# Performance work log

Hardware: AMD Instinct MI355X
Metric: run time of the kernel (lower is better)

Reference implementation:

```python
import jax, jax.numpy as jnp
import numpy as np

B, S, D, H = 1, 2048, 4096, 32
HD = D // H
THETA = 10000.0
IN_SCALE = 0.1   # input_scale buffer
Q_SCALE = 0.1    # q_proj_scale buffer
K_SCALE = 0.1    # k_proj_scale buffer
V_SCALE = 0.1    # v_proj_scale buffer
OUT_SCALE = 0.1  # out_input_scale buffer


def _fake_q(x, scale, lo, hi):
    # round-to-int + clamp, kept in float (faithful to int8 fake-quant)
    return jnp.clip(jnp.round(x / scale), lo, hi)


def _w4a8_linear(x, qw, w_scale, in_scale):
    # int8 fake-quantized activation x int4-valued weight, dequant output
    qx = _fake_q(x, in_scale, -128, 127)
    return jnp.einsum('bsd,od->bso', qx, qw) * (in_scale * w_scale)


def _rope_tables(position_ids):
    inv_freq = 1.0 / (THETA ** (jnp.arange(0, HD, 2, dtype=jnp.float32) / HD))
    ang = position_ids.astype(jnp.float32)[..., None] * inv_freq  # [B,S,HD/2]
    emb = jnp.concatenate([ang, ang], axis=-1)                     # [B,S,HD]
    return jnp.cos(emb)[:, None], jnp.sin(emb)[:, None]            # [B,1,S,HD]


def _rotate_half(x):
    return jnp.concatenate([-x[..., HD // 2:], x[..., :HD // 2]], axis=-1)


def setup_inputs() -> dict:
    key = jax.random.key(0)
    ks = jax.random.split(key, 9)
    hidden_states = jax.random.normal(ks[0], (B, S, D), jnp.float32)
    def int4_w(k):
        return jnp.round(jax.random.uniform(k, (D, D), jnp.float32, -8.0, 7.0))
    def ch_scale(k):
        return jax.random.uniform(k, (D,), jnp.float32, 0.01, 0.03)
    wq, wk, wv, wo = int4_w(ks[1]), int4_w(ks[2]), int4_w(ks[3]), int4_w(ks[4])
    sq_w, sk_w, sv_w, so_w = ch_scale(ks[5]), ch_scale(ks[6]), ch_scale(ks[7]), ch_scale(ks[8])
    position_ids = jnp.arange(S, dtype=jnp.int32)[None, :]
    causal = jnp.tril(jnp.ones((S, S), dtype=bool))
    attention_mask = jnp.where(causal, 0.0, -1e9).astype(jnp.float32)[None, None]
    return dict(hidden_states=hidden_states, wq=wq, wk=wk, wv=wv, wo=wo,
                sq_w=sq_w, sk_w=sk_w, sv_w=sv_w, so_w=so_w,
                attention_mask=attention_mask, position_ids=position_ids)


def reference(hidden_states, wq, wk, wv, wo, sq_w, sk_w, sv_w, so_w,
              attention_mask, position_ids):
    # W4A8 dequant projections
    q = _w4a8_linear(hidden_states, wq, sq_w, IN_SCALE)
    k = _w4a8_linear(hidden_states, wk, sk_w, IN_SCALE)
    v = _w4a8_linear(hidden_states, wv, sv_w, IN_SCALE)
    q = q.reshape(B, S, H, HD).transpose(0, 2, 1, 3)  # [B,H,S,HD]
    k = k.reshape(B, S, H, HD).transpose(0, 2, 1, 3)
    v = v.reshape(B, S, H, HD).transpose(0, 2, 1, 3)
    # RoPE
    cos, sin = _rope_tables(position_ids)
    q = q * cos + _rotate_half(q) * sin
    k = k * cos + _rotate_half(k) * sin
    # int8 fake-quant of q/k/v, then dequant before matmuls
    q = _fake_q(q, Q_SCALE, -128, 127)
    k = _fake_q(k, K_SCALE, -128, 127)
    v = _fake_q(v, V_SCALE, -128, 127)
    scores = jnp.einsum('bhqd,bhkd->bhqk', q * Q_SCALE, k * K_SCALE) / np.sqrt(HD)
    scores = scores + attention_mask
    attn = jax.nn.softmax(scores.astype(jnp.float32), axis=-1)
    out = jnp.einsum('bhqk,bhkd->bhqd', attn, v * V_SCALE)
    out = out.transpose(0, 2, 1, 3).reshape(B, S, D)
    # o_proj input re-quantized to int8 with out_input_scale (clamp -127..127)
    out_q = _fake_q(out, OUT_SCALE, -127, 127)
    attn_output = jnp.einsum('bsd,od->bso', out_q, wo) * (OUT_SCALE * so_w)
    return attn_output
```

## Files before the change

### kernel.cpp

```cpp
#include <hip/hip_runtime.h>
#include <math.h>
#include <stdint.h>

#define S_LEN 2048
#define D_DIM 4096
#define NHEAD 32
#define HDIM  128

typedef int      v4i __attribute__((ext_vector_type(4)));
typedef float    v4f __attribute__((ext_vector_type(4)));
typedef _Float16 v8h __attribute__((ext_vector_type(8)));

__device__ __forceinline__ float quant128(float x) {
  return fminf(fmaxf(rintf(x / 0.1f), -128.f), 127.f);
}
__device__ __forceinline__ void gl_lds16(const void* g, void* l) {
  __builtin_amdgcn_global_load_lds(
      (const __attribute__((address_space(1))) void*)g,
      (__attribute__((address_space(3))) void*)l, 16, 0, 0);
}

__global__ __launch_bounds__(256) void quant_hidden_k(const float* __restrict__ in,
                                                      int8_t* __restrict__ out) {
  const int idx = blockIdx.x * 256 + threadIdx.x;
  const float4 v = ((const float4*)in)[idx];
  const int q0 = (int)quant128(v.x), q1 = (int)quant128(v.y);
  const int q2 = (int)quant128(v.z), q3 = (int)quant128(v.w);
  ((int*)out)[idx] = (q0 & 0xff) | ((q1 & 0xff) << 8) | ((q2 & 0xff) << 16) | ((q3 & 0xff) << 24);
}

__global__ __launch_bounds__(256) void wconv3_k(const float* __restrict__ a,
                                                const float* __restrict__ b,
                                                const float* __restrict__ c,
                                                int8_t* __restrict__ out) {
  const int which = blockIdx.x >> 14;
  const int sub = blockIdx.x & 16383;
  const float* src = (which == 0) ? a : (which == 1) ? b : c;
  const int idx = sub * 256 + threadIdx.x;
  const float4 v = ((const float4*)src)[idx];
  const int q0 = __float2int_rn(v.x), q1 = __float2int_rn(v.y);
  const int q2 = __float2int_rn(v.z), q3 = __float2int_rn(v.w);
  ((int*)out)[(size_t)which * 4194304 + idx] =
      (q0 & 0xff) | ((q1 & 0xff) << 8) | ((q2 & 0xff) << 16) | ((q3 & 0xff) << 24);
}

__global__ __launch_bounds__(256) void wconv_k(const float* __restrict__ in,
                                               int8_t* __restrict__ out) {
  const int idx = blockIdx.x * 256 + threadIdx.x;
  const float4 v = ((const float4*)in)[idx];
  const int q0 = __float2int_rn(v.x), q1 = __float2int_rn(v.y);
  const int q2 = __float2int_rn(v.z), q3 = __float2int_rn(v.w);
  ((int*)out)[idx] = (q0 & 0xff) | ((q1 & 0xff) << 8) | ((q2 & 0xff) << 16) | ((q3 & 0xff) << 24);
}

__global__ __launch_bounds__(256) void rope_tab_k(const int* __restrict__ pos,
                                                  float* __restrict__ ct,
                                                  float* __restrict__ st) {
  const int idx = blockIdx.x * 256 + threadIdx.x;
  const int s = idx >> 6, j = idx & 63;
  const float inv = exp2f((float)j * -0.20762050593046016f);
  const float a = (float)pos[s] * inv;
  float si, c;
  sincosf(a, &si, &c);
  ct[idx] = c;
  st[idx] = si;
}

template <int MODE>
__device__ __forceinline__ void gemm_body(
    int8_t* __restrict__ LS, const int8_t* __restrict__ A8,
    const int8_t* __restrict__ W8, const float* __restrict__ s0,
    const float* __restrict__ s1, const float* __restrict__ s2,
    const float* __restrict__ ctab, const float* __restrict__ stab,
    void* __restrict__ out0, void* __restrict__ out1, void* __restrict__ out2,
    int nwg) {
  int8_t* const Abase = LS;
  int8_t* const Bbase = LS + 49152;

  const int t = threadIdx.x;
  const int w = t >> 6, lane = t & 63, g = lane >> 4, l15 = lane & 15;
  const int wm = w >> 2, wn = w & 3;

  const int bid = blockIdx.x;
  const int lb = (bid & 7) * (nwg >> 3) + (bid >> 3);
  const int within = lb & 15, g16 = lb >> 4;
  const int bm = ((g16 & 3) * 4 + (within >> 2)) * 128;
  const int bn = ((g16 >> 2) * 4 + (within & 3)) * 256;

  const int rowo = lane >> 3;
  const int schunk = ((lane & 7) ^ rowo) * 16;
  const int8_t* srcA[2];
  const int8_t* srcB[4];
#pragma unroll
  for (int i = 0; i < 2; ++i)
    srcA[i] = A8 + (size_t)(bm + w * 16 + i * 8 + rowo) * D_DIM + schunk;
#pragma unroll
  for (int i = 0; i < 4; ++i)
    srcB[i] = W8 + (size_t)(bn + w * 32 + i * 8 + rowo) * D_DIM + schunk;

#define STAGE(KT, BI)                                                       \
  {                                                                         \
    const int kof_ = (KT) * 128;                                            \
    int8_t* Ad_ = Abase + (BI) * 16384 + w * 2048;                          \
    int8_t* Bd_ = Bbase + (BI) * 32768 + w * 4096;                          \
    _Pragma("unroll") for (int i_ = 0; i_ < 2; ++i_)                        \
        gl_lds16(srcA[i_] + kof_, Ad_ + i_ * 1024);                         \
    _Pragma("unroll") for (int i_ = 0; i_ < 4; ++i_)                        \
        gl_lds16(srcB[i_] + kof_, Bd_ + i_ * 1024);                         \
  }

  const int nc0 = (wn & 1) * 32 + (wn >> 1) * 128;

  const int coff0 = (g ^ (l15 & 7)) * 16;
  const int coff1 = ((4 | g) ^ (l15 & 7)) * 16;
  const int aoff = (wm * 64 + l15) * 128;
  int boff[4];
#pragma unroll
  for (int ni = 0; ni < 4; ++ni)
    boff[ni] = (nc0 + (ni & 1) * 16 + (ni >> 1) * 64 + l15) * 128;

  v4i fa[4], fb[4];
  v4i ga[4], gb[4];

#define RD(FA, FB, BI, COFF)                                                \
  {                                                                         \
    const int8_t* Ab_ = Abase + (BI) * 16384;                               \
    const int8_t* Bb_ = Bbase + (BI) * 32768;                               \
    _Pragma("unroll") for (int mi_ = 0; mi_ < 4; ++mi_)                     \
        FA[mi_] = *(const v4i*)(Ab_ + aoff + mi_ * 2048 + (COFF));          \
    _Pragma("unroll") for (int ni_ = 0; ni_ < 4; ++ni_)                     \
        FB[ni_] = *(const v4i*)(Bb_ + boff[ni_] + (COFF));                  \
  }

#define MM(FA, FB)                                                          \
  _Pragma("unroll") for (int mi_ = 0; mi_ < 4; ++mi_)                       \
  _Pragma("unroll") for (int ni_ = 0; ni_ < 4; ++ni_)                       \
      acc[mi_][ni_] = __builtin_amdgcn_mfma_i32_16x16x64_i8(                \
          FA[mi_], FB[ni_], acc[mi_][ni_], 0, 0, 0);

  v4i acc[4][4];
#pragma unroll
  for (int mi = 0; mi < 4; ++mi)
#pragma unroll
    for (int ni = 0; ni < 4; ++ni) acc[mi][ni] = (v4i){0, 0, 0, 0};

  STAGE(0, 0)
  STAGE(1, 1)
  asm volatile("s_waitcnt vmcnt(6)" ::: "memory");
  __builtin_amdgcn_s_barrier();
  __builtin_amdgcn_sched_barrier(0);
  RD(fa, fb, 0, coff0)

  for (int t3 = 0; t3 < 33; t3 += 3) {
#pragma unroll
    for (int u = 0; u < 3; ++u) {
      const int kt = t3 + u;
      if (kt < 32) {
        if (kt + 2 < 32) STAGE(kt + 2, ((u + 2) % 3))
        RD(ga, gb, u, coff1)
        __builtin_amdgcn_s_setprio(1);
        MM(fa, fb)
        MM(ga, gb)
        __builtin_amdgcn_s_setprio(0);
        if (kt + 2 < 32)
          asm volatile("s_waitcnt vmcnt(6)" ::: "memory");
        else
          asm volatile("s_waitcnt vmcnt(0)" ::: "memory");
        __builtin_amdgcn_s_barrier();
        __builtin_amdgcn_sched_barrier(0);
        if (kt + 1 < 32) RD(fa, fb, ((u + 1) % 3), coff0)
      }
    }
  }
#undef STAGE
#undef RD
#undef MM

  const int srow0 = bm + wm * 64;
  if (MODE == 1) {
    float* dst = (float*)out0;
#pragma unroll
    for (int ni = 0; ni < 4; ++ni) {
      const int col = bn + nc0 + (ni & 1) * 16 + (ni >> 1) * 64 + l15;
      const float sc = 0.1f * s0[col];
#pragma unroll
      for (int mi = 0; mi < 4; ++mi)
#pragma unroll
        for (int r = 0; r < 4; ++r)
          dst[(size_t)(srow0 + mi * 16 + g * 4 + r) * D_DIM + col] =
              (float)acc[mi][ni][r] * sc;
    }
  } else {
    const int seg = bn >> 12;
    const int bcol = bn & 4095;
    if (seg == 2) {
      _Float16* dst = (_Float16*)out2;
#pragma unroll
      for (int ni = 0; ni < 4; ++ni) {
        const int col = bcol + nc0 + (ni & 1) * 16 + (ni >> 1) * 64 + l15;
        const float scv = 0.1f * s2[col];
#pragma unroll
        for (int mi = 0; mi < 4; ++mi)
#pragma unroll
          for (int r = 0; r < 4; ++r) {
            const int s = srow0 + mi * 16 + g * 4 + r;
            dst[(size_t)col * S_LEN + s] = (_Float16)quant128((float)acc[mi][ni][r] * scv);
          }
      }
    } else {
      const float* wsc = seg ? s1 : s0;
      int8_t* dst = seg ? (int8_t*)out1 : (int8_t*)out0;
      const int hb = bcol + (wn >> 1) * 128;
#pragma unroll
      for (int ni = 0; ni < 2; ++ni) {
        const int dlo = (wn & 1) * 32 + ni * 16 + l15;
        const int clo = hb + dlo;
        const float sc0 = 0.1f * wsc[clo];
        const float sc1 = 0.1f * wsc[clo + 64];
#pragma unroll
        for (int mi = 0; mi < 4; ++mi)
#pragma unroll
          for (int r = 0; r < 4; ++r) {
            const int s = srow0 + mi * 16 + g * 4 + r;
            const float c = ctab[s * 64 + dlo];
            const float si = stab[s * 64 + dlo];
            const float x1 = (float)acc[mi][ni][r] * sc0;
            const float x2 = (float)acc[mi][ni + 2][r] * sc1;
            dst[(size_t)s * D_DIM + clo] = (int8_t)quant128(x1 * c - x2 * si);
            dst[(size_t)s * D_DIM + clo + 64] = (int8_t)quant128(x2 * c + x1 * si);
          }
      }
    }
  }
}

__global__ __launch_bounds__(512) void gemm_qkv(
    const int8_t* __restrict__ A8, const int8_t* __restrict__ W8,
    const float* __restrict__ s0, const float* __restrict__ s1,
    const float* __restrict__ s2, const float* __restrict__ ctab,
    const float* __restrict__ stab, void* __restrict__ out0,
    void* __restrict__ out1, void* __restrict__ out2) {
  __shared__ __align__(16) int8_t LS[3 * 16384 + 3 * 32768];
  gemm_body<0>(LS, A8, W8, s0, s1, s2, ctab, stab, out0, out1, out2, 768);
}

__global__ __launch_bounds__(512) void gemm_out(
    const int8_t* __restrict__ A8, const int8_t* __restrict__ W8,
    const float* __restrict__ s0, const float* __restrict__ ctab,
    const float* __restrict__ stab, void* __restrict__ out0) {
  __shared__ __align__(16) int8_t LS[3 * 16384 + 3 * 32768];
  gemm_body<1>(LS, A8, W8, s0, s0, s0, ctab, stab, out0, out0, out0, 256);
}

__global__ __launch_bounds__(512, 4) void attn_v8(
    const int8_t* __restrict__ q8, const int8_t* __restrict__ k8,
    const _Float16* __restrict__ vT, int8_t* __restrict__ o8) {
  __shared__ __align__(16) int8_t Kls[3][8192];
  __shared__ __align__(16) int8_t Vls[3][16384];
  const int jj = 15 - blockIdx.x;
  const int h = blockIdx.y;
  const int t = threadIdx.x;
  const int w = t >> 6, lane = t & 63, g = lane >> 4, l15 = lane & 15;
  const int T = 2 * jj + 2;
  const int q0 = (jj * 8 + w) * 16;
  const int q_lane = q0 + l15;
  const float SSCALE = 8.838834764831845e-4f;
  const v8h vones = {(_Float16)1, (_Float16)1, (_Float16)1, (_Float16)1,
                     (_Float16)1, (_Float16)1, (_Float16)1, (_Float16)1};

  const int ks_slot = t >> 3;
  const int ks_cs = (t & 7) ^ (ks_slot & 7);
  const int ks_key = ((ks_slot >> 5) & 1) * 32 + ((ks_slot >> 3) & 1) * 16 +
                     ((ks_slot >> 2) & 1) * 8 + ((ks_slot >> 4) & 1) * 4 +
                     (ks_slot & 3);
  const int k_src = ks_key * D_DIM + ks_cs * 16;
  const int k_dst = t * 16;
  int v_src[2], v_dst[2];
#pragma unroll
  for (int i = 0; i < 2; ++i) {
    const int lin = i * 512 + t;
    const int d = lin >> 3;
    const int cs = (lin & 7) ^ (d & 7);
    v_src[i] = d * S_LEN + cs * 8;
    v_dst[i] = lin * 16;
  }
  const int8_t* kbg = k8 + (size_t)h * HDIM;
  const _Float16* vbg = vT + (size_t)h * HDIM * S_LEN;

  auto stage = [&](int kt, int b) {
    const int8_t* ks = kbg + (size_t)kt * (64 * D_DIM);
    const _Float16* vs = vbg + kt * 64;
    gl_lds16(ks + k_src, &Kls[b][k_dst]);
#pragma unroll
    for (int i = 0; i < 2; ++i) gl_lds16(vs + v_src[i], &Vls[b][v_dst[i]]);
  };

  const v4i qa0 = *(const v4i*)(q8 + (size_t)q_lane * D_DIM + h * HDIM + g * 16);
  const v4i qa1 = *(const v4i*)(q8 + (size_t)q_lane * D_DIM + h * HDIM + 64 + g * 16);

  v4f o[8];
#pragma unroll
  for (int n = 0; n < 8; ++n) o[n] = (v4f){0.f, 0.f, 0.f, 0.f};
  v4f lacc = (v4f){0.f, 0.f, 0.f, 0.f};
  float m_i = -INFINITY;

  stage(0, 0);
  if (T > 1) stage(1, 1);

  int bi = 0;
  for (int kt = 0; kt < T; ++kt) {
    if (kt + 1 < T)
      asm volatile("s_waitcnt vmcnt(3)" ::: "memory");
    else
      asm volatile("s_waitcnt vmcnt(0)" ::: "memory");
    __builtin_amdgcn_s_barrier();
    __builtin_amdgcn_sched_barrier(0);
    if (kt + 2 < T) stage(kt + 2, bi >= 1 ? bi - 1 : bi + 2);

    const int ksw = (l15 & 7);
    float sc[4][4];
#pragma unroll
    for (int nt = 0; nt < 4; ++nt) {
      const int8_t* kr = &Kls[bi][(nt * 16 + l15) * 128];
      const v4i kb0 = *(const v4i*)(kr + ((g ^ ksw) * 16));
      const v4i kb1 = *(const v4i*)(kr + (((4 + g) ^ ksw) * 16));
      v4i c = (v4i){0, 0, 0, 0};
      c = __builtin_amdgcn_mfma_i32_16x16x64_i8(kb0, qa0, c, 0, 0, 0);
      c = __builtin_amdgcn_mfma_i32_16x16x64_i8(kb1, qa1, c, 0, 0, 0);
#pragma unroll
      for (int r = 0; r < 4; ++r) {
        float s = (float)c[r] * SSCALE;
        if (kt >= T - 2) {
          const int key = kt * 64 + ((nt >> 1) << 5) + ((g >> 1) << 4) +
                          ((g & 1) << 3) + ((nt & 1) << 2) + r;
          if (key > q_lane) s = -1.0e30f;
        }
        sc[nt][r] = s;
      }
    }
    float mx = fmaxf(fmaxf(fmaxf(sc[0][0], sc[0][1]), fmaxf(sc[0][2], sc[0][3])),
                     fmaxf(fmaxf(sc[1][0], sc[1][1]), fmaxf(sc[1][2], sc[1][3])));
    mx = fmaxf(mx, fmaxf(fmaxf(fmaxf(sc[2][0], sc[2][1]), fmaxf(sc[2][2], sc[2][3])),
                         fmaxf(fmaxf(sc[3][0], sc[3][1]), fmaxf(sc[3][2], sc[3][3]))));
    mx = fmaxf(mx, __shfl_xor(mx, 16));
    mx = fmaxf(mx, __shfl_xor(mx, 32));
    const float mnew = fmaxf(m_i, mx);
    const float alpha = __expf(m_i - mnew);
    m_i = mnew;

    float p[4][4];
#pragma unroll
    for (int nt = 0; nt < 4; ++nt)
#pragma unroll
      for (int r = 0; r < 4; ++r) p[nt][r] = __expf(sc[nt][r] - m_i);

    v8h ph0, ph1;
#pragma unroll
    for (int e = 0; e < 8; ++e) {
      ph0[e] = (_Float16)p[e >> 2][e & 3];
      ph1[e] = (_Float16)p[2 + (e >> 2)][e & 3];
    }
    float a_r[4];
#pragma unroll
    for (int r = 0; r < 4; ++r)
      a_r[r] = __shfl(alpha, (lane & 48) | (g * 4 + r));
#pragma unroll
    for (int n = 0; n < 8; ++n)
#pragma unroll
      for (int r = 0; r < 4; ++r) o[n][r] *= a_r[r];
#pragma unroll
    for (int r = 0; r < 4; ++r) lacc[r] *= a_r[r];

    __builtin_amdgcn_s_setprio(1);
    lacc = __builtin_amdgcn_mfma_f32_16x16x32_f16(ph0, vones, lacc, 0, 0, 0);
    lacc = __builtin_amdgcn_mfma_f32_16x16x32_f16(ph1, vones, lacc, 0, 0, 0);
#pragma unroll
    for (int nt = 0; nt < 8; ++nt) {
      const int8_t* vr = &Vls[bi][(nt * 16 + l15) * 128];
      const v8h v0 = *(const v8h*)(vr + ((g ^ ksw) * 16));
      const v8h v1 = *(const v8h*)(vr + (((4 + g) ^ ksw) * 16));
      o[nt] = __builtin_amdgcn_mfma_f32_16x16x32_f16(ph0, v0, o[nt], 0, 0, 0);
      o[nt] = __builtin_amdgcn_mfma_f32_16x16x32_f16(ph1, v1, o[nt], 0, 0, 0);
    }
    __builtin_amdgcn_s_setprio(0);

    bi = (bi == 2) ? 0 : bi + 1;
  }

#pragma unroll
  for (int r = 0; r < 4; ++r) {
    const float rL = 1.0f / lacc[r];
    const size_t row = (size_t)(q0 + g * 4 + r) * D_DIM + h * HDIM;
#pragma unroll
    for (int nt = 0; nt < 8; ++nt) {
      const int q = (int)fminf(fmaxf(rintf(o[nt][r] * rL), -127.f), 127.f);
      o8[row + nt * 16 + l15] = (int8_t)q;
    }
  }
}

extern "C" void kernel_launch(void* const* d_in, const int* in_sizes, int n_in,
                              void* d_out, int out_size, void* d_ws, size_t ws_size,
                              hipStream_t stream) {
  (void)in_sizes; (void)n_in; (void)out_size; (void)ws_size;
  const float* hidden = (const float*)d_in[0];
  const float* wq = (const float*)d_in[1];
  const float* wk = (const float*)d_in[2];
  const float* wv = (const float*)d_in[3];
  const float* wo = (const float*)d_in[4];
  const float* sq = (const float*)d_in[5];
  const float* sk = (const float*)d_in[6];
  const float* sv = (const float*)d_in[7];
  const float* so = (const float*)d_in[8];
  const int* pos = (const int*)d_in[10];
  float* out = (float*)d_out;

  char* ws = (char*)d_ws;
  int8_t* h8 = (int8_t*)ws;
  int8_t* q8 = (int8_t*)(ws + (8ull << 20));
  int8_t* k8 = (int8_t*)(ws + (16ull << 20));
  _Float16* vT = (_Float16*)(ws + (24ull << 20));
  int8_t* w8a = (int8_t*)(ws + (40ull << 20));
  int8_t* w8b = (int8_t*)(ws + (56ull << 20));
  int8_t* w8c = (int8_t*)(ws + (72ull << 20));
  float* ctab = (float*)(ws + (88ull << 20));
  float* stab = (float*)(ws + (88ull << 20) + (512ull << 10));
  int8_t* o8 = h8;

  hipLaunchKernelGGL(rope_tab_k, dim3(512), dim3(256), 0, stream, pos, ctab, stab);
  hipLaunchKernelGGL(quant_hidden_k, dim3(8192), dim3(256), 0, stream, hidden, h8);
  hipLaunchKernelGGL(wconv3_k, dim3(49152), dim3(256), 0, stream, wq, wk, wv, w8a);

  hipLaunchKernelGGL(gemm_qkv, dim3(768), dim3(512), 0, stream, h8, w8a,
                     sq, sk, sv, ctab, stab, (void*)q8, (void*)k8, (void*)vT);
  hipLaunchKernelGGL(wconv_k, dim3(16384), dim3(256), 0, stream, wo, w8a);
  hipLaunchKernelGGL(attn_v8, dim3(16, 32), dim3(512), 0, stream, q8, k8, vT, o8);
  hipLaunchKernelGGL(gemm_out, dim3(256), dim3(512), 0, stream, o8, w8a,
                     so, ctab, stab, (void*)out);
}
```

Baseline: 505.2 us.

## Enlarge GEMM tiles to 256x256 with 64-wide K steps and new LDS swizzle

```diff
diff --git a/kernel.cpp b/kernel.cpp
--- a/kernel.cpp
+++ b/kernel.cpp
@@ -84,99 +84,88 @@
   const int bid = blockIdx.x;
   const int lb = (bid & 7) * (nwg >> 3) + (bid >> 3);
   const int within = lb & 15, g16 = lb >> 4;
-  const int bm = ((g16 & 3) * 4 + (within >> 2)) * 128;
-  const int bn = ((g16 >> 2) * 4 + (within & 3)) * 256;
-
-  const int rowo = lane >> 3;
-  const int schunk = ((lane & 7) ^ rowo) * 16;
+  const int bm = ((g16 & 1) * 4 + (within >> 2)) * 256;
+  const int bn = ((g16 >> 1) * 4 + (within & 3)) * 256;
+
   const int8_t* srcA[2];
-  const int8_t* srcB[4];
-#pragma unroll
-  for (int i = 0; i < 2; ++i)
-    srcA[i] = A8 + (size_t)(bm + w * 16 + i * 8 + rowo) * D_DIM + schunk;
-#pragma unroll
-  for (int i = 0; i < 4; ++i)
-    srcB[i] = W8 + (size_t)(bn + w * 32 + i * 8 + rowo) * D_DIM + schunk;
+  const int8_t* srcB[2];
+  int sdst[2];
+#pragma unroll
+  for (int i = 0; i < 2; ++i) {
+    const int lin = i * 512 + t;
+    const int row = lin >> 2;
+    const int sc = (lin & 3) ^ ((row >> 1) & 3);
+    srcA[i] = A8 + (size_t)(bm + row) * D_DIM + sc * 16;
+    srcB[i] = W8 + (size_t)(bn + row) * D_DIM + sc * 16;
+    sdst[i] = lin * 16;
+  }
 
 #define STAGE(KT, BI)                                                       \
   {                                                                         \
-    const int kof_ = (KT) * 128;                                            \
-    int8_t* Ad_ = Abase + (BI) * 16384 + w * 2048;                          \
-    int8_t* Bd_ = Bbase + (BI) * 32768 + w * 4096;                          \
-    _Pragma("unroll") for (int i_ = 0; i_ < 2; ++i_)                        \
-        gl_lds16(srcA[i_] + kof_, Ad_ + i_ * 1024);                         \
-    _Pragma("unroll") for (int i_ = 0; i_ < 4; ++i_)                        \
-        gl_lds16(srcB[i_] + kof_, Bd_ + i_ * 1024);                         \
-  }
-
+    const int kof_ = (KT) * 64;                                             \
+    _Pragma("unroll") for (int i_ = 0; i_ < 2; ++i_) {                      \
+      gl_lds16(srcA[i_] + kof_, Abase + (BI) * 16384 + sdst[i_]);           \
+      gl_lds16(srcB[i_] + kof_, Bbase + (BI) * 16384 + sdst[i_]);           \
+    }                                                                       \
+  }
+
+  const int cg = ((g ^ ((l15 >> 1) & 3)) << 4);
   const int nc0 = (wn & 1) * 32 + (wn >> 1) * 128;
-
-  const int coff0 = (g ^ (l15 & 7)) * 16;
-  const int coff1 = ((4 | g) ^ (l15 & 7)) * 16;
-  const int aoff = (wm * 64 + l15) * 128;
-  int boff[4];
+  int aoffs[8], boffs[4];
+#pragma unroll
+  for (int mi = 0; mi < 8; ++mi)
+    aoffs[mi] = (wm * 128 + mi * 16 + l15) * 64 + cg;
 #pragma unroll
   for (int ni = 0; ni < 4; ++ni)
-    boff[ni] = (nc0 + (ni & 1) * 16 + (ni >> 1) * 64 + l15) * 128;
-
-  v4i fa[4], fb[4];
-  v4i ga[4], gb[4];
-
-#define RD(FA, FB, BI, COFF)                                                \
-  {                                                                         \
-    const int8_t* Ab_ = Abase + (BI) * 16384;                               \
-    const int8_t* Bb_ = Bbase + (BI) * 32768;                               \
-    _Pragma("unroll") for (int mi_ = 0; mi_ < 4; ++mi_)                     \
-        FA[mi_] = *(const v4i*)(Ab_ + aoff + mi_ * 2048 + (COFF));          \
-    _Pragma("unroll") for (int ni_ = 0; ni_ < 4; ++ni_)                     \
-        FB[ni_] = *(const v4i*)(Bb_ + boff[ni_] + (COFF));                  \
-  }
-
-#define MM(FA, FB)                                                          \
-  _Pragma("unroll") for (int mi_ = 0; mi_ < 4; ++mi_)                       \
-  _Pragma("unroll") for (int ni_ = 0; ni_ < 4; ++ni_)                       \
-      acc[mi_][ni_] = __builtin_amdgcn_mfma_i32_16x16x64_i8(                \
-          FA[mi_], FB[ni_], acc[mi_][ni_], 0, 0, 0);
-
-  v4i acc[4][4];
-#pragma unroll
-  for (int mi = 0; mi < 4; ++mi)
+    boffs[ni] = (nc0 + (ni & 1) * 16 + (ni >> 1) * 64 + l15) * 64 + cg;
+
+  v4i acc[8][4];
+#pragma unroll
+  for (int mi = 0; mi < 8; ++mi)
 #pragma unroll
     for (int ni = 0; ni < 4; ++ni) acc[mi][ni] = (v4i){0, 0, 0, 0};
 
   STAGE(0, 0)
   STAGE(1, 1)
-  asm volatile("s_waitcnt vmcnt(6)" ::: "memory");
+  asm volatile("s_waitcnt vmcnt(4)" ::: "memory");
   __builtin_amdgcn_s_barrier();
   __builtin_amdgcn_sched_barrier(0);
-  RD(fa, fb, 0, coff0)
-
-  for (int t3 = 0; t3 < 33; t3 += 3) {
+
+  for (int t3 = 0; t3 < 66; t3 += 3) {
 #pragma unroll
     for (int u = 0; u < 3; ++u) {
       const int kt = t3 + u;
-      if (kt < 32) {
-        if (kt + 2 < 32) STAGE(kt + 2, ((u + 2) % 3))
-        RD(ga, gb, u, coff1)
+      if (kt < 64) {
+        if (kt + 2 < 64) STAGE(kt + 2, ((u + 2) % 3))
+        v4i af[8], bf[4];
+        {
+          const int8_t* Ab_ = Abase + u * 16384;
+          const int8_t* Bb_ = Bbase + u * 16384;
+#pragma unroll
+          for (int mi = 0; mi < 8; ++mi) af[mi] = *(const v4i*)(Ab_ + aoffs[mi]);
+#pragma unroll
+          for (int ni = 0; ni < 4; ++ni) bf[ni] = *(const v4i*)(Bb_ + boffs[ni]);
+        }
         __builtin_amdgcn_s_setprio(1);
-        MM(fa, fb)
-        MM(ga, gb)
+#pragma unroll
+        for (int mi = 0; mi < 8; ++mi)
+#pragma unroll
+          for (int ni = 0; ni < 4; ++ni)
+            acc[mi][ni] = __builtin_amdgcn_mfma_i32_16x16x64_i8(
+                af[mi], bf[ni], acc[mi][ni], 0, 0, 0);
         __builtin_amdgcn_s_setprio(0);
-        if (kt + 2 < 32)
-          asm volatile("s_waitcnt vmcnt(6)" ::: "memory");
+        if (kt + 2 < 64)
+          asm volatile("s_waitcnt vmcnt(4)" ::: "memory");
         else
           asm volatile("s_waitcnt vmcnt(0)" ::: "memory");
         __builtin_amdgcn_s_barrier();
         __builtin_amdgcn_sched_barrier(0);
-        if (kt + 1 < 32) RD(fa, fb, ((u + 1) % 3), coff0)
       }
     }
   }
 #undef STAGE
-#undef RD
-#undef MM
-
-  const int srow0 = bm + wm * 64;
+
+  const int srow0 = bm + wm * 128;
   if (MODE == 1) {
     float* dst = (float*)out0;
 #pragma unroll
@@ -184,7 +173,7 @@
       const int col = bn + nc0 + (ni & 1) * 16 + (ni >> 1) * 64 + l15;
       const float sc = 0.1f * s0[col];
 #pragma unroll
-      for (int mi = 0; mi < 4; ++mi)
+      for (int mi = 0; mi < 8; ++mi)
 #pragma unroll
         for (int r = 0; r < 4; ++r)
           dst[(size_t)(srow0 + mi * 16 + g * 4 + r) * D_DIM + col] =
@@ -200,7 +189,7 @@
         const int col = bcol + nc0 + (ni & 1) * 16 + (ni >> 1) * 64 + l15;
         const float scv = 0.1f * s2[col];
 #pragma unroll
-        for (int mi = 0; mi < 4; ++mi)
+        for (int mi = 0; mi < 8; ++mi)
 #pragma unroll
           for (int r = 0; r < 4; ++r) {
             const int s = srow0 + mi * 16 + g * 4 + r;
@@ -218,7 +207,7 @@
         const float sc0 = 0.1f * wsc[clo];
         const float sc1 = 0.1f * wsc[clo + 64];
 #pragma unroll
-        for (int mi = 0; mi < 4; ++mi)
+        for (int mi = 0; mi < 8; ++mi)
 #pragma unroll
           for (int r = 0; r < 4; ++r) {
             const int s = srow0 + mi * 16 + g * 4 + r;
@@ -240,16 +229,16 @@
     const float* __restrict__ s2, const float* __restrict__ ctab,
     const float* __restrict__ stab, void* __restrict__ out0,
     void* __restrict__ out1, void* __restrict__ out2) {
-  __shared__ __align__(16) int8_t LS[3 * 16384 + 3 * 32768];
-  gemm_body<0>(LS, A8, W8, s0, s1, s2, ctab, stab, out0, out1, out2, 768);
+  __shared__ __align__(16) int8_t LS[6 * 16384];
+  gemm_body<0>(LS, A8, W8, s0, s1, s2, ctab, stab, out0, out1, out2, 384);
 }
 
 __global__ __launch_bounds__(512) void gemm_out(
     const int8_t* __restrict__ A8, const int8_t* __restrict__ W8,
     const float* __restrict__ s0, const float* __restrict__ ctab,
     const float* __restrict__ stab, void* __restrict__ out0) {
-  __shared__ __align__(16) int8_t LS[3 * 16384 + 3 * 32768];
-  gemm_body<1>(LS, A8, W8, s0, s0, s0, ctab, stab, out0, out0, out0, 256);
+  __shared__ __align__(16) int8_t LS[6 * 16384];
+  gemm_body<1>(LS, A8, W8, s0, s0, s0, ctab, stab, out0, out0, out0, 128);
 }
 
 __global__ __launch_bounds__(512, 4) void attn_v8(
@@ -431,10 +420,10 @@
   hipLaunchKernelGGL(quant_hidden_k, dim3(8192), dim3(256), 0, stream, hidden, h8);
   hipLaunchKernelGGL(wconv3_k, dim3(49152), dim3(256), 0, stream, wq, wk, wv, w8a);
 
-  hipLaunchKernelGGL(gemm_qkv, dim3(768), dim3(512), 0, stream, h8, w8a,
+  hipLaunchKernelGGL(gemm_qkv, dim3(384), dim3(512), 0, stream, h8, w8a,
                      sq, sk, sv, ctab, stab, (void*)q8, (void*)k8, (void*)vT);
   hipLaunchKernelGGL(wconv_k, dim3(16384), dim3(256), 0, stream, wo, w8a);
   hipLaunchKernelGGL(attn_v8, dim3(16, 32), dim3(512), 0, stream, q8, k8, vT, o8);
-  hipLaunchKernelGGL(gemm_out, dim3(256), dim3(512), 0, stream, o8, w8a,
+  hipLaunchKernelGGL(gemm_out, dim3(128), dim3(512), 0, stream, o8, w8a,
                      so, ctab, stab, (void*)out);
 }
```

Result: slower. 557.3 us (+10.3%).
